# Kernel optimization log

Measured on AMD Instinct MI355X. Metric: run time of the kernel, lower is better.

Reference implementation:

```python
import jax, jax.numpy as jnp
import numpy as np

B, T, F, H, L = 256, 512, 64, 256, 2
DH = 2 * H          # decoder hidden size (bidirectional encoder concat)
OUT, OSL = 2, 20    # output_size, output_seq_len


def gru_cell(x, h, Wih, Whh, bih, bhh):
    # PyTorch GRU cell, gate order (r, z, n)
    gi = x @ Wih.T + bih
    gh = h @ Whh.T + bhh
    ir, iz, inn = jnp.split(gi, 3, axis=-1)
    hr, hz, hn = jnp.split(gh, 3, axis=-1)
    r = jax.nn.sigmoid(ir + hr)
    z = jax.nn.sigmoid(iz + hz)
    n = jnp.tanh(inn + r * hn)
    return (1.0 - z) * n + z * h


def setup_inputs() -> dict:
    key = jax.random.key(0)
    ks = iter(jax.random.split(key, 32))
    def p(shape, scale=0.05):
        return jax.random.normal(next(ks), shape, dtype=jnp.float32) * scale
    inp = {
        "x": p((B, T, F), 1.0),
        "start_token": jnp.zeros((1, 1, OUT), jnp.float32),
        # encoder layer 0 (input F), layer 1 (input 2H); axis 0 = direction (fwd, bwd)
        "enc_Wih0": p((2, 3 * H, F)), "enc_Whh0": p((2, 3 * H, H)),
        "enc_bih0": p((2, 3 * H)),   "enc_bhh0": p((2, 3 * H)),
        "enc_Wih1": p((2, 3 * H, 2 * H)), "enc_Whh1": p((2, 3 * H, H)),
        "enc_bih1": p((2, 3 * H)),   "enc_bhh1": p((2, 3 * H)),
        # decoder: unidirectional, hidden DH; layer0 input OUT, layer1 input DH
        "dec_Wih0": p((3 * DH, OUT)), "dec_Whh0": p((3 * DH, DH)),
        "dec_bih0": p((3 * DH,)),    "dec_bhh0": p((3 * DH,)),
        "dec_Wih1": p((3 * DH, DH)), "dec_Whh1": p((3 * DH, DH)),
        "dec_bih1": p((3 * DH,)),    "dec_bhh1": p((3 * DH,)),
        "fc_W": p((OUT, DH)), "fc_b": p((OUT,)),
    }
    return inp


def _run_dir(xs, Wih, Whh, bih, bhh, reverse):
    # xs: [T, B, Fin] -> (ys [T, B, H], h_T [B, H])
    h0 = jnp.zeros((xs.shape[1], Whh.shape[1]), xs.dtype)
    def step(h, xt):
        hn = gru_cell(xt, h, Wih, Whh, bih, bhh)
        return hn, hn
    hT, ys = jax.lax.scan(step, h0, xs, reverse=reverse)
    return ys, hT


def reference(x, start_token,
              enc_Wih0, enc_Whh0, enc_bih0, enc_bhh0,
              enc_Wih1, enc_Whh1, enc_bih1, enc_bhh1,
              dec_Wih0, dec_Whh0, dec_bih0, dec_bhh0,
              dec_Wih1, dec_Whh1, dec_bih1, dec_bhh1,
              fc_W, fc_b):
    b = x.shape[0]
    xs = jnp.swapaxes(x, 0, 1)  # [T, B, F]
    enc_layers = [(enc_Wih0, enc_Whh0, enc_bih0, enc_bhh0),
                  (enc_Wih1, enc_Whh1, enc_bih1, enc_bhh1)]
    hiddens = []
    layer_in = xs
    for (Wih, Whh, bih, bhh) in enc_layers:
        yf, hf = _run_dir(layer_in, Wih[0], Whh[0], bih[0], bhh[0], reverse=False)
        yb, hb = _run_dir(layer_in, Wih[1], Whh[1], bih[1], bhh[1], reverse=True)
        layer_in = jnp.concatenate([yf, yb], axis=-1)   # [T, B, 2H]
        hiddens.append(jnp.concatenate([hf, hb], axis=-1))  # [B, 2H] = cat(fwd, bwd)
    inp0 = jnp.broadcast_to(start_token, (b, 1, OUT))[:, 0]  # [B, OUT]
    def dec_step(carry, _):
        inp, (h0, h1) = carry
        h0n = gru_cell(inp, h0, dec_Wih0, dec_Whh0, dec_bih0, dec_bhh0)
        h1n = gru_cell(h0n, h1, dec_Wih1, dec_Whh1, dec_bih1, dec_bhh1)
        pred = h1n @ fc_W.T + fc_b
        return (pred, (h0n, h1n)), pred
    _, preds = jax.lax.scan(dec_step, (inp0, (hiddens[0], hiddens[1])), None, length=OSL)
    return jnp.swapaxes(preds, 0, 1)  # [B, OSL, OUT]
```

## Files before the change

### kernel.cpp

```cpp
#include <hip/hip_runtime.h>
#include <hip/hip_bf16.h>
#include <stdint.h>
#include <stddef.h>


typedef __bf16 bf16_t;
typedef bf16_t bf16x8 __attribute__((ext_vector_type(8)));
typedef float  f32x4  __attribute__((ext_vector_type(4)));

#define B_   256
#define T_   512
#define F_   64
#define H_   256
#define G_   768
#define DH_  512
#define DG_  1536
#define OSL_ 20

__device__ __forceinline__ float sigm(float x) {
    float e = __builtin_amdgcn_exp2f(-1.442695040888963f * x);
    return __builtin_amdgcn_rcpf(1.0f + e);
}
__device__ __forceinline__ float tanh_(float x) {
    float e = __builtin_amdgcn_exp2f(-2.885390081777927f * x);
    return __builtin_amdgcn_rcpf(1.0f + e) * 2.0f - 1.0f;
}

__device__ __forceinline__ bf16x8 load_f32x8_as_bf16(const float* p) {
    f32x4 u = *(const f32x4*)p;
    f32x4 v = *(const f32x4*)(p + 4);
    bf16x8 r;
    r[0]=(bf16_t)u[0]; r[1]=(bf16_t)u[1]; r[2]=(bf16_t)u[2]; r[3]=(bf16_t)u[3];
    r[4]=(bf16_t)v[0]; r[5]=(bf16_t)v[1]; r[6]=(bf16_t)v[2]; r[7]=(bf16_t)v[3];
    return r;
}

__global__ __launch_bounds__(256) void prep_all(
    const float* __restrict__ s0, const float* __restrict__ s1,
    const float* __restrict__ s2, const float* __restrict__ s3,
    const float* __restrict__ s4, const float* __restrict__ s5,
    const float* __restrict__ s6,
    bf16_t* __restrict__ d0, bf16_t* __restrict__ d1, bf16_t* __restrict__ d2,
    bf16_t* __restrict__ d3, bf16_t* __restrict__ d4, bf16_t* __restrict__ d5,
    bf16_t* __restrict__ d6,
    const float* __restrict__ wih0d, const float* __restrict__ fcw,
    const float* __restrict__ fcb, const float* __restrict__ bih0d,
    const float* __restrict__ st, bf16_t* __restrict__ weff,
    float* __restrict__ beff, float* __restrict__ ov,
    unsigned int* __restrict__ bar) {
    int i = blockIdx.x * 256 + threadIdx.x;
    switch (blockIdx.y) {
      case 0: if (i < 2*G_*F_)  d0[i] = (bf16_t)s0[i]; break;
      case 1: if (i < 2*G_*H_)  d1[i] = (bf16_t)s1[i]; break;
      case 2: if (i < 2*G_*DH_) d2[i] = (bf16_t)s2[i]; break;
      case 3: if (i < 2*G_*H_)  d3[i] = (bf16_t)s3[i]; break;
      case 4: if (i < DG_*DH_)  d4[i] = (bf16_t)s4[i]; break;
      case 5: if (i < DG_*DH_)  d5[i] = (bf16_t)s5[i]; break;
      case 6: if (i < DG_*DH_)  d6[i] = (bf16_t)s6[i]; break;
      default: {
        if (i < 1024) bar[i] = 0u;
        if (i < DG_*DH_) {
          int g = i >> 9, k = i & 511;
          float a0 = wih0d[g * 2], a1 = wih0d[g * 2 + 1];
          weff[i] = (bf16_t)(a0 * fcw[k] + a1 * fcw[DH_ + k]);
          if (k == 0) {
            beff[g] = a0 * fcb[0] + a1 * fcb[1] + bih0d[g];
            ov[g]   = a0 * st[0]  + a1 * st[1]  + bih0d[g];
          }
        }
      } break;
    }
}

__global__ __launch_bounds__(256) void gemm_gi(
    const float* __restrict__ x, const bf16_t* __restrict__ xcat,
    const bf16_t* __restrict__ Bt, bf16_t* __restrict__ gi, int t0, int K) {
    __shared__ bf16_t As[128 * 64];
    __shared__ bf16_t Bs[128 * 64];
    int m0 = blockIdx.x * 128, n0 = blockIdx.y * 128;
    int tid = threadIdx.x;
    int lane = tid & 63, w = tid >> 6;
    int col = lane & 15, quad = lane >> 4;
    int qm = (w >> 1) * 64, qn = (w & 1) * 64;

    int tl = m0 >> 8;
    int bbase = m0 & 255;
    int t_real = t0 + tl;
    if (n0 >= 768) t_real = (T_ - 1) - t_real;

    f32x4 acc[4][4] = {};
    for (int k0 = 0; k0 < K; k0 += 64) {
        __syncthreads();
#pragma unroll
        for (int i = 0; i < 4; i++) {
            int c = i * 256 + tid;
            int m = c >> 3, kc = c & 7;
            int kcs = kc ^ (m & 7);
            bf16x8 av;
            if (K == 64) {
                av = load_f32x8_as_bf16(x + ((size_t)(bbase + m) * T_ + t_real) * F_ + kcs * 8);
            } else {
                av = *(const bf16x8*)(xcat + ((size_t)t_real * B_ + bbase + m) * DH_ + k0 + kcs * 8);
            }
            *(bf16x8*)(&As[c * 8]) = av;
            *(bf16x8*)(&Bs[c * 8]) = *(const bf16x8*)(Bt + (size_t)(n0 + m) * K + k0 + kcs * 8);
        }
        __syncthreads();
#pragma unroll
        for (int kt = 0; kt < 2; kt++) {
            bf16x8 a[4], b[4];
#pragma unroll
            for (int mt = 0; mt < 4; mt++) {
                int r = qm + mt * 16 + col;
                a[mt] = *(const bf16x8*)(&As[(r * 8 + ((kt * 4 + quad) ^ (r & 7))) * 8]);
                int rn = qn + mt * 16 + col;
                b[mt] = *(const bf16x8*)(&Bs[(rn * 8 + ((kt * 4 + quad) ^ (rn & 7))) * 8]);
            }
#pragma unroll
            for (int mt = 0; mt < 4; mt++)
#pragma unroll
                for (int nt = 0; nt < 4; nt++)
                    acc[mt][nt] = __builtin_amdgcn_mfma_f32_16x16x32_bf16(a[mt], b[nt], acc[mt][nt], 0, 0, 0);
        }
    }
#pragma unroll
    for (int mt = 0; mt < 4; mt++)
#pragma unroll
        for (int nt = 0; nt < 4; nt++)
#pragma unroll
            for (int i = 0; i < 4; i++) {
                int row = m0 + qm + mt * 16 + quad * 4 + i;
                int cg  = n0 + qn + nt * 16 + col;
                gi[(size_t)row * DG_ + cg] = (bf16_t)acc[mt][nt][i];
            }
}

__global__ __launch_bounds__(512) void gru_scan(
    const bf16_t* __restrict__ gi, int t0, int tc,
    const bf16_t* __restrict__ whh,
    const float* __restrict__ bih, const float* __restrict__ bhh,
    float* __restrict__ hstate, bf16_t* __restrict__ y, float* __restrict__ hT) {
    __shared__ bf16_t gi_lds[16 * 768];
    __shared__ bf16_t h_lds[2 * 16 * 264];

    int dir = blockIdx.x >> 4;
    int b0  = (blockIdx.x & 15) * 16;
    int tid = threadIdx.x;
    int w = tid >> 6, lane = tid & 63, col = lane & 15, quad = lane >> 4;

    bf16x8 wf[3][2][8];
    const bf16_t* wbase = whh + (size_t)dir * G_ * H_;
#pragma unroll
    for (int g = 0; g < 3; g++)
#pragma unroll
        for (int nt = 0; nt < 2; nt++) {
            int row = g * 256 + w * 32 + nt * 16 + col;
#pragma unroll
            for (int kt = 0; kt < 8; kt++)
                wf[g][nt][kt] = *(const bf16x8*)(wbase + (size_t)row * H_ + kt * 32 + quad * 8);
        }
    float brz[2][2], bin_[2], bhn[2];
#pragma unroll
    for (int nt = 0; nt < 2; nt++) {
        int j = w * 32 + nt * 16 + col;
        brz[0][nt] = bih[dir * G_ + j] + bhh[dir * G_ + j];
        brz[1][nt] = bih[dir * G_ + 256 + j] + bhh[dir * G_ + 256 + j];
        bin_[nt]   = bih[dir * G_ + 512 + j];
        bhn[nt]    = bhh[dir * G_ + 512 + j];
    }
    int bb[3], oo[3];
#pragma unroll
    for (int it = 0; it < 3; it++) {
        int c = it * 512 + tid;
        bb[it] = c / 96;
        oo[it] = (c % 96) * 8;
    }
    float hold[2][4];
#pragma unroll
    for (int nt = 0; nt < 2; nt++)
#pragma unroll
        for (int i = 0; i < 4; i++) {
            int j = w * 32 + nt * 16 + col;
            hold[nt][i] = t0 ? hstate[dir * 65536 + (b0 + quad * 4 + i) * 256 + j] : 0.0f;
        }
    for (int i = tid; i < 16 * 264; i += 512) {
        int b = i / 264, j = i % 264;
        float v = (t0 && j < 256) ? hstate[dir * 65536 + (b0 + b) * 256 + j] : 0.0f;
        h_lds[i] = (bf16_t)v;
    }
#pragma unroll
    for (int it = 0; it < 3; it++) {
        int c = it * 512 + tid;
        *(bf16x8*)(&gi_lds[c * 8]) =
            *(const bf16x8*)(gi + ((size_t)0 * B_ + b0 + bb[it]) * DG_ + dir * G_ + oo[it]);
    }
    __syncthreads();

    for (int s = 0; s < tc; s++) {
        int par = s & 1;
        int t = t0 + s;
        int sn = (s + 1 < tc) ? (s + 1) : s;

        bf16x8 pg[3];
#pragma unroll
        for (int it = 0; it < 3; it++)
            pg[it] = *(const bf16x8*)(gi + ((size_t)sn * B_ + b0 + bb[it]) * DG_ + dir * G_ + oo[it]);

        f32x4 acc[3][2] = {};
        const bf16_t* hcur = &h_lds[par * 4224];
#pragma unroll
        for (int kt = 0; kt < 8; kt++) {
            bf16x8 af = *(const bf16x8*)(hcur + col * 264 + kt * 32 + quad * 8);
#pragma unroll
            for (int g = 0; g < 3; g++)
#pragma unroll
                for (int nt = 0; nt < 2; nt++)
                    acc[g][nt] = __builtin_amdgcn_mfma_f32_16x16x32_bf16(af, wf[g][nt][kt], acc[g][nt], 0, 0, 0);
        }

        bf16_t* hnext = &h_lds[(par ^ 1) * 4224];
        int tp = dir ? (T_ - 1 - t) : t;
#pragma unroll
        for (int nt = 0; nt < 2; nt++) {
            int j = w * 32 + nt * 16 + col;
#pragma unroll
            for (int i = 0; i < 4; i++) {
                int b = quad * 4 + i;
                float gr = acc[0][nt][i] + (float)gi_lds[b * 768 + j]       + brz[0][nt];
                float gz = acc[1][nt][i] + (float)gi_lds[b * 768 + 256 + j] + brz[1][nt];
                float gn = (float)gi_lds[b * 768 + 512 + j] + bin_[nt];
                float r = sigm(gr), z = sigm(gz);
                float n = tanh_(gn + r * (acc[2][nt][i] + bhn[nt]));
                float hv = (1.0f - z) * n + z * hold[nt][i];
                hold[nt][i] = hv;
                hnext[b * 264 + j] = (bf16_t)hv;
                if (t == T_ - 1) hT[(size_t)(b0 + b) * DH_ + dir * H_ + j] = hv;
            }
        }
        __syncthreads();
        if (y) {
            int b = tid >> 5, seg = tid & 31;
            *(bf16x8*)(y + ((size_t)tp * B_ + b0 + b) * DH_ + dir * H_ + seg * 8) =
                *(const bf16x8*)(&h_lds[(par ^ 1) * 4224 + b * 264 + seg * 8]);
        }
#pragma unroll
        for (int it = 0; it < 3; it++)
            *(bf16x8*)(&gi_lds[(it * 512 + tid) * 8]) = pg[it];
        __syncthreads();
    }
#pragma unroll
    for (int nt = 0; nt < 2; nt++)
#pragma unroll
        for (int i = 0; i < 4; i++) {
            int j = w * 32 + nt * 16 + col;
            hstate[dir * 65536 + (b0 + quad * 4 + i) * 256 + j] = hold[nt][i];
        }
}


__device__ __forceinline__ void gbar(unsigned int* cnt) {
    __syncthreads();
    if (threadIdx.x == 0) {
        __hip_atomic_fetch_add(cnt, 1u, __ATOMIC_RELEASE, __HIP_MEMORY_SCOPE_AGENT);
        unsigned int s = 0;
        while (__hip_atomic_load(cnt, __ATOMIC_RELAXED, __HIP_MEMORY_SCOPE_AGENT) < 8u
               && ++s < (1u << 20))
            __builtin_amdgcn_s_sleep(2);
    }
    __syncthreads();
}

__device__ __forceinline__ void stage16(bf16_t* lds, const bf16_t* src) {
    const char* s = (const char*)src;
    char* d = (char*)lds;
#pragma unroll
    for (int i2 = 0; i2 < 8; ++i2) {
        int off = i2 * 2048 + threadIdx.x * 8;
        unsigned long long v = __hip_atomic_load(
            (const unsigned long long*)(s + off),
            __ATOMIC_RELAXED, __HIP_MEMORY_SCOPE_AGENT);
        int row = off >> 10;
        int swz = off ^ ((row & 7) << 4);
        *(unsigned long long*)(d + swz) = v;
    }
}

__device__ __forceinline__ bf16x8 fragrd(const bf16_t* lds, int kt, int col, int quad) {
    int byte = (col * 1024 + kt * 64 + quad * 16) ^ ((col & 7) << 4);
    return *(const bf16x8*)((const char*)lds + byte);
}

__device__ __forceinline__ void publish(bf16_t* dst, int b, int j, float hv, int col) {
    bf16_t hb = (bf16_t)hv;
    unsigned short mb;
    __builtin_memcpy(&mb, &hb, 2);
    unsigned int pv = (unsigned int)__shfl_xor((int)(unsigned int)mb, 1);
    if ((col & 1) == 0) {
        unsigned int word = (unsigned int)mb | (pv << 16);
        __hip_atomic_store((unsigned int*)((char*)dst + (size_t)(b * DH_ + j) * 2),
                           word, __ATOMIC_RELAXED, __HIP_MEMORY_SCOPE_AGENT);
    }
}

__device__ __forceinline__ void cell_step(
    const bf16_t* sh, const bf16_t* sx, bool dox,
    const bf16_t* __restrict__ Wx, const bf16_t* __restrict__ Wh,
    int j, int col, int quad, int grp,
    float br, float bz, float bin_, float bhn,
    float hold[4], bf16_t* hout, float* hist_t) {
    f32x4 aR = {}, aZ = {}, aIN = {}, aHN = {};
#pragma unroll
    for (int kt = 0; kt < 16; ++kt) {
        bf16x8 ah = fragrd(sh, kt, col, quad);
        bf16x8 w0 = *(const bf16x8*)(Wh + (size_t)j * DH_ + kt * 32 + quad * 8);
        bf16x8 w1 = *(const bf16x8*)(Wh + (size_t)(DH_ + j) * DH_ + kt * 32 + quad * 8);
        bf16x8 w2 = *(const bf16x8*)(Wh + (size_t)(2 * DH_ + j) * DH_ + kt * 32 + quad * 8);
        aR  = __builtin_amdgcn_mfma_f32_16x16x32_bf16(ah, w0, aR, 0, 0, 0);
        aZ  = __builtin_amdgcn_mfma_f32_16x16x32_bf16(ah, w1, aZ, 0, 0, 0);
        aHN = __builtin_amdgcn_mfma_f32_16x16x32_bf16(ah, w2, aHN, 0, 0, 0);
        if (dox) {
            bf16x8 ax = fragrd(sx, kt, col, quad);
            bf16x8 x0 = *(const bf16x8*)(Wx + (size_t)j * DH_ + kt * 32 + quad * 8);
            bf16x8 x1 = *(const bf16x8*)(Wx + (size_t)(DH_ + j) * DH_ + kt * 32 + quad * 8);
            bf16x8 x2 = *(const bf16x8*)(Wx + (size_t)(2 * DH_ + j) * DH_ + kt * 32 + quad * 8);
            aR  = __builtin_amdgcn_mfma_f32_16x16x32_bf16(ax, x0, aR, 0, 0, 0);
            aZ  = __builtin_amdgcn_mfma_f32_16x16x32_bf16(ax, x1, aZ, 0, 0, 0);
            aIN = __builtin_amdgcn_mfma_f32_16x16x32_bf16(ax, x2, aIN, 0, 0, 0);
        }
    }
#pragma unroll
    for (int i = 0; i < 4; ++i) {
        int b = grp * 16 + quad * 4 + i;
        float r = sigm(aR[i] + br);
        float z = sigm(aZ[i] + bz);
        float n = tanh_(aIN[i] + bin_ + r * (aHN[i] + bhn));
        float hv = (1.0f - z) * n + z * hold[i];
        hold[i] = hv;
        if (hist_t) hist_t[(size_t)b * DH_ + j] = hv;
        publish(hout, b, j, hv, col);
    }
}

__global__ __launch_bounds__(256) void dec_persist(
    const bf16_t* __restrict__ weff, const float* __restrict__ beff,
    const float* __restrict__ ov,
    const bf16_t* __restrict__ wdhh0, const float* __restrict__ dbhh0,
    const bf16_t* __restrict__ wdih1, const float* __restrict__ dbih1,
    const bf16_t* __restrict__ wdhh1, const float* __restrict__ dbhh1,
    const float* __restrict__ h0init, const float* __restrict__ h1init,
    bf16_t* hx00, bf16_t* hx01, bf16_t* hx10, bf16_t* hx11,
    float* __restrict__ hist, unsigned int* __restrict__ bar) {
    __shared__ bf16_t sh[16 * 512];
    __shared__ bf16_t sx[16 * 512];
    int jblk = blockIdx.x & 7;
    int grp  = blockIdx.x >> 3;
    int tid = threadIdx.x, w = tid >> 6, lane = tid & 63;
    int col = lane & 15, quad = lane >> 4;
    int j = jblk * 64 + w * 16 + col;

    float b0r = beff[j] + dbhh0[j],           b0z = beff[DH_ + j] + dbhh0[DH_ + j];
    float b0in = beff[2 * DH_ + j],           b0hn = dbhh0[2 * DH_ + j];
    float o0r = ov[j] + dbhh0[j],             o0z = ov[DH_ + j] + dbhh0[DH_ + j];
    float o0in = ov[2 * DH_ + j];
    float b1r = dbih1[j] + dbhh1[j],          b1z = dbih1[DH_ + j] + dbhh1[DH_ + j];
    float b1in = dbih1[2 * DH_ + j],          b1hn = dbhh1[2 * DH_ + j];

    float hold0[4], hold1[4];
#pragma unroll
    for (int i = 0; i < 4; ++i) {
        int b = grp * 16 + quad * 4 + i;
        float v0 = h0init[(size_t)b * DH_ + j];
        float v1 = h1init[(size_t)b * DH_ + j];
        hold0[i] = v0; hold1[i] = v1;
        publish(hx01, b, j, v0, col);
        publish(hx11, b, j, v1, col);
    }
    gbar(bar + grp);

    int ph = 1;
    for (int t = 0; t < OSL_; ++t) {
        bf16_t* write0 = (t & 1) ? hx01 : hx00;
        bf16_t* read0  = (t & 1) ? hx00 : hx01;
        bf16_t* write1 = (t & 1) ? hx11 : hx10;
        bf16_t* read1  = (t & 1) ? hx10 : hx11;

        bool dox0 = (t > 0);
        __syncthreads();
        stage16(sh, read0 + (size_t)grp * 16 * DH_);
        if (dox0) stage16(sx, read1 + (size_t)grp * 16 * DH_);
        __syncthreads();
        cell_step(sh, sx, dox0, weff, wdhh0, j, col, quad, grp,
                  dox0 ? b0r : o0r, dox0 ? b0z : o0z, dox0 ? b0in : o0in, b0hn,
                  hold0, write0, nullptr);
        gbar(bar + ph * 16 + grp); ph++;

        __syncthreads();
        stage16(sh, read1 + (size_t)grp * 16 * DH_);
        stage16(sx, write0 + (size_t)grp * 16 * DH_);
        __syncthreads();
        cell_step(sh, sx, true, wdih1, wdhh1, j, col, quad, grp,
                  b1r, b1z, b1in, b1hn,
                  hold1, write1, hist + (size_t)t * B_ * DH_);
        gbar(bar + ph * 16 + grp); ph++;
    }
}

__global__ __launch_bounds__(256) void fc_all(
    const float* __restrict__ hist, const float* __restrict__ fcw,
    const float* __restrict__ fcb, float* __restrict__ out) {
    int t  = blockIdx.x >> 4;
    int b0 = (blockIdx.x & 15) * 16;
    int tid = threadIdx.x;
    int bl = tid >> 4, o = (tid >> 3) & 1, part = tid & 7;
    const float* hp = hist + ((size_t)t * B_ + b0 + bl) * DH_;
    const float* wp = fcw + o * DH_;
    float s = 0.0f;
    for (int k = part * 64; k < part * 64 + 64; k += 4) {
        f32x4 hv = *(const f32x4*)(hp + k);
        f32x4 wv = *(const f32x4*)(wp + k);
        s += hv[0] * wv[0] + hv[1] * wv[1] + hv[2] * wv[2] + hv[3] * wv[3];
    }
    s += __shfl_down(s, 4); s += __shfl_down(s, 2); s += __shfl_down(s, 1);
    if (part == 0) out[(size_t)(b0 + bl) * (OSL_ * 2) + t * 2 + o] = s + fcb[o];
}


#define OFF_WIH0E 0ull
#define OFF_WHH0E 196608ull
#define OFF_WIH1E 983040ull
#define OFF_WHH1E 2555904ull
#define OFF_WDHH0 3342336ull
#define OFF_WDIH1 4915200ull
#define OFF_WDHH1 6488064ull
#define OFF_WEFF  8060928ull
#define OFF_BEFF  9633792ull
#define OFF_BAR   9641984ull
#define OFF_OV    9658368ull
#define OFF_H0A   9682944ull
#define OFF_H0B   10207232ull
#define OFF_H1A   10731520ull
#define OFF_H1B   11255808ull
#define OFF_HST   11780096ull
#define OFF_HIST  12304384ull
#define OFF_XCAT  22790144ull
#define OFF_GI    157007872ull

extern "C" void kernel_launch(void* const* d_in, const int* in_sizes, int n_in,
                              void* d_out, int out_size, void* d_ws, size_t ws_size,
                              hipStream_t stream) {
    const float* x      = (const float*)d_in[0];
    const float* st     = (const float*)d_in[1];
    const float* eWih0  = (const float*)d_in[2];
    const float* eWhh0  = (const float*)d_in[3];
    const float* ebih0  = (const float*)d_in[4];
    const float* ebhh0  = (const float*)d_in[5];
    const float* eWih1  = (const float*)d_in[6];
    const float* eWhh1  = (const float*)d_in[7];
    const float* ebih1  = (const float*)d_in[8];
    const float* ebhh1  = (const float*)d_in[9];
    const float* dWih0  = (const float*)d_in[10];
    const float* dWhh0  = (const float*)d_in[11];
    const float* dbih0  = (const float*)d_in[12];
    const float* dbhh0  = (const float*)d_in[13];
    const float* dWih1  = (const float*)d_in[14];
    const float* dWhh1  = (const float*)d_in[15];
    const float* dbih1  = (const float*)d_in[16];
    const float* dbhh1  = (const float*)d_in[17];
    const float* fcW    = (const float*)d_in[18];
    const float* fcb    = (const float*)d_in[19];

    char* ws = (char*)d_ws;
    bf16_t* wih0e = (bf16_t*)(ws + OFF_WIH0E);
    bf16_t* whh0e = (bf16_t*)(ws + OFF_WHH0E);
    bf16_t* wih1e = (bf16_t*)(ws + OFF_WIH1E);
    bf16_t* whh1e = (bf16_t*)(ws + OFF_WHH1E);
    bf16_t* wdhh0 = (bf16_t*)(ws + OFF_WDHH0);
    bf16_t* wdih1 = (bf16_t*)(ws + OFF_WDIH1);
    bf16_t* wdhh1 = (bf16_t*)(ws + OFF_WDHH1);
    bf16_t* weff  = (bf16_t*)(ws + OFF_WEFF);
    float*  beff  = (float*)(ws + OFF_BEFF);
    unsigned int* bar = (unsigned int*)(ws + OFF_BAR);
    float*  ovp   = (float*)(ws + OFF_OV);
    float*  h0init = (float*)(ws + OFF_H0A);
    float*  h1init = (float*)(ws + OFF_H1A);
    bf16_t* hx00  = (bf16_t*)(ws + OFF_H0B);
    bf16_t* hx01  = (bf16_t*)(ws + OFF_H0B + 262144ull);
    bf16_t* hx10  = (bf16_t*)(ws + OFF_H1B);
    bf16_t* hx11  = (bf16_t*)(ws + OFF_H1B + 262144ull);
    float*  hstate = (float*)(ws + OFF_HST);
    float*  hist  = (float*)(ws + OFF_HIST);
    bf16_t* xcat  = (bf16_t*)(ws + OFF_XCAT);
    bf16_t* gi    = (bf16_t*)(ws + OFF_GI);

    int Tc = 512;
    while (Tc > 8 && OFF_GI + (unsigned long long)Tc * 786432ull > (unsigned long long)ws_size)
        Tc >>= 1;
    int nch = T_ / Tc;

    prep_all<<<dim3(3072, 8), 256, 0, stream>>>(
        eWih0, eWhh0, eWih1, eWhh1, dWhh0, dWih1, dWhh1,
        wih0e, whh0e, wih1e, whh1e, wdhh0, wdih1, wdhh1,
        dWih0, fcW, fcb, dbih0, st, weff, beff, ovp, bar);

    for (int c = 0; c < nch; c++) {
        gemm_gi<<<dim3(Tc * 2, 12), 256, 0, stream>>>(x, nullptr, wih0e, gi, c * Tc, 64);
        gru_scan<<<32, 512, 0, stream>>>(gi, c * Tc, Tc, whh0e, ebih0, ebhh0, hstate, xcat, h0init);
    }
    for (int c = 0; c < nch; c++) {
        gemm_gi<<<dim3(Tc * 2, 12), 256, 0, stream>>>(nullptr, xcat, wih1e, gi, c * Tc, 512);
        gru_scan<<<32, 512, 0, stream>>>(gi, c * Tc, Tc, whh1e, ebih1, ebhh1, hstate, nullptr, h1init);
    }

    dec_persist<<<128, 256, 0, stream>>>(weff, beff, ovp,
                                         wdhh0, dbhh0, wdih1, dbih1, wdhh1, dbhh1,
                                         h0init, h1init,
                                         hx00, hx01, hx10, hx11,
                                         hist, bar);

    fc_all<<<OSL_ * 16, 256, 0, stream>>>(hist, fcW, fcb, (float*)d_out);
}
```

Baseline: 5.067 ms.

## Hoist decoder layer-1 recurrent GEMM before barrier, swap GEMM grid axes, direct y stores

In the decoder, the layer-1 recurrent product (h1 times Whh1) only depends on the previous step, so it is now computed together with layer 0 before the first grid barrier. This shortens the critical path between barriers and drops one LDS staging of h1. The gi GEMM grid swaps its x and y axes so the N tiles vary fastest, which changes the block order for cache reuse of the A tiles. The encoder scan now writes y directly from registers as scalar bf16 stores instead of vectorized copies out of LDS, and the barrier spin sleep is shortened. Scalar scattered stores may use more memory transactions than the old vector copies.

```diff
diff --git a/kernel.cpp b/kernel.cpp
--- a/kernel.cpp
+++ b/kernel.cpp
@@ -77,7 +77,7 @@
     const bf16_t* __restrict__ Bt, bf16_t* __restrict__ gi, int t0, int K) {
     __shared__ bf16_t As[128 * 64];
     __shared__ bf16_t Bs[128 * 64];
-    int m0 = blockIdx.x * 128, n0 = blockIdx.y * 128;
+    int m0 = blockIdx.y * 128, n0 = blockIdx.x * 128;
     int tid = threadIdx.x;
     int lane = tid & 63, w = tid >> 6;
     int col = lane & 15, quad = lane >> 4;
@@ -234,15 +234,11 @@
                 float hv = (1.0f - z) * n + z * hold[nt][i];
                 hold[nt][i] = hv;
                 hnext[b * 264 + j] = (bf16_t)hv;
+                if (y) y[((size_t)tp * B_ + b0 + b) * DH_ + dir * H_ + j] = (bf16_t)hv;
                 if (t == T_ - 1) hT[(size_t)(b0 + b) * DH_ + dir * H_ + j] = hv;
             }
         }
         __syncthreads();
-        if (y) {
-            int b = tid >> 5, seg = tid & 31;
-            *(bf16x8*)(y + ((size_t)tp * B_ + b0 + b) * DH_ + dir * H_ + seg * 8) =
-                *(const bf16x8*)(&h_lds[(par ^ 1) * 4224 + b * 264 + seg * 8]);
-        }
 #pragma unroll
         for (int it = 0; it < 3; it++)
             *(bf16x8*)(&gi_lds[(it * 512 + tid) * 8]) = pg[it];
@@ -265,7 +261,7 @@
         unsigned int s = 0;
         while (__hip_atomic_load(cnt, __ATOMIC_RELAXED, __HIP_MEMORY_SCOPE_AGENT) < 8u
                && ++s < (1u << 20))
-            __builtin_amdgcn_s_sleep(2);
+            __builtin_amdgcn_s_sleep(1);
     }
     __syncthreads();
 }
@@ -299,45 +295,6 @@
         unsigned int word = (unsigned int)mb | (pv << 16);
         __hip_atomic_store((unsigned int*)((char*)dst + (size_t)(b * DH_ + j) * 2),
                            word, __ATOMIC_RELAXED, __HIP_MEMORY_SCOPE_AGENT);
-    }
-}
-
-__device__ __forceinline__ void cell_step(
-    const bf16_t* sh, const bf16_t* sx, bool dox,
-    const bf16_t* __restrict__ Wx, const bf16_t* __restrict__ Wh,
-    int j, int col, int quad, int grp,
-    float br, float bz, float bin_, float bhn,
-    float hold[4], bf16_t* hout, float* hist_t) {
-    f32x4 aR = {}, aZ = {}, aIN = {}, aHN = {};
-#pragma unroll
-    for (int kt = 0; kt < 16; ++kt) {
-        bf16x8 ah = fragrd(sh, kt, col, quad);
-        bf16x8 w0 = *(const bf16x8*)(Wh + (size_t)j * DH_ + kt * 32 + quad * 8);
-        bf16x8 w1 = *(const bf16x8*)(Wh + (size_t)(DH_ + j) * DH_ + kt * 32 + quad * 8);
-        bf16x8 w2 = *(const bf16x8*)(Wh + (size_t)(2 * DH_ + j) * DH_ + kt * 32 + quad * 8);
-        aR  = __builtin_amdgcn_mfma_f32_16x16x32_bf16(ah, w0, aR, 0, 0, 0);
-        aZ  = __builtin_amdgcn_mfma_f32_16x16x32_bf16(ah, w1, aZ, 0, 0, 0);
-        aHN = __builtin_amdgcn_mfma_f32_16x16x32_bf16(ah, w2, aHN, 0, 0, 0);
-        if (dox) {
-            bf16x8 ax = fragrd(sx, kt, col, quad);
-            bf16x8 x0 = *(const bf16x8*)(Wx + (size_t)j * DH_ + kt * 32 + quad * 8);
-            bf16x8 x1 = *(const bf16x8*)(Wx + (size_t)(DH_ + j) * DH_ + kt * 32 + quad * 8);
-            bf16x8 x2 = *(const bf16x8*)(Wx + (size_t)(2 * DH_ + j) * DH_ + kt * 32 + quad * 8);
-            aR  = __builtin_amdgcn_mfma_f32_16x16x32_bf16(ax, x0, aR, 0, 0, 0);
-            aZ  = __builtin_amdgcn_mfma_f32_16x16x32_bf16(ax, x1, aZ, 0, 0, 0);
-            aIN = __builtin_amdgcn_mfma_f32_16x16x32_bf16(ax, x2, aIN, 0, 0, 0);
-        }
-    }
-#pragma unroll
-    for (int i = 0; i < 4; ++i) {
-        int b = grp * 16 + quad * 4 + i;
-        float r = sigm(aR[i] + br);
-        float z = sigm(aZ[i] + bz);
-        float n = tanh_(aIN[i] + bin_ + r * (aHN[i] + bhn));
-        float hv = (1.0f - z) * n + z * hold[i];
-        hold[i] = hv;
-        if (hist_t) hist_t[(size_t)b * DH_ + j] = hv;
-        publish(hout, b, j, hv, col);
     }
 }
 
@@ -383,24 +340,79 @@
         bf16_t* read0  = (t & 1) ? hx00 : hx01;
         bf16_t* write1 = (t & 1) ? hx11 : hx10;
         bf16_t* read1  = (t & 1) ? hx10 : hx11;
-
         bool dox0 = (t > 0);
+
         __syncthreads();
         stage16(sh, read0 + (size_t)grp * 16 * DH_);
-        if (dox0) stage16(sx, read1 + (size_t)grp * 16 * DH_);
-        __syncthreads();
-        cell_step(sh, sx, dox0, weff, wdhh0, j, col, quad, grp,
-                  dox0 ? b0r : o0r, dox0 ? b0z : o0z, dox0 ? b0in : o0in, b0hn,
-                  hold0, write0, nullptr);
+        stage16(sx, read1 + (size_t)grp * 16 * DH_);
+        __syncthreads();
+
+        f32x4 aR0 = {}, aZ0 = {}, aHN0 = {}, aIN0 = {};
+        f32x4 aR1 = {}, aZ1 = {}, aHN1 = {};
+#pragma unroll
+        for (int kt = 0; kt < 16; ++kt) {
+            bf16x8 ah = fragrd(sh, kt, col, quad);
+            bf16x8 ax = fragrd(sx, kt, col, quad);
+            bf16x8 h0w0 = *(const bf16x8*)(wdhh0 + (size_t)j * DH_ + kt * 32 + quad * 8);
+            bf16x8 h0w1 = *(const bf16x8*)(wdhh0 + (size_t)(DH_ + j) * DH_ + kt * 32 + quad * 8);
+            bf16x8 h0w2 = *(const bf16x8*)(wdhh0 + (size_t)(2 * DH_ + j) * DH_ + kt * 32 + quad * 8);
+            aR0  = __builtin_amdgcn_mfma_f32_16x16x32_bf16(ah, h0w0, aR0, 0, 0, 0);
+            aZ0  = __builtin_amdgcn_mfma_f32_16x16x32_bf16(ah, h0w1, aZ0, 0, 0, 0);
+            aHN0 = __builtin_amdgcn_mfma_f32_16x16x32_bf16(ah, h0w2, aHN0, 0, 0, 0);
+            bf16x8 h1w0 = *(const bf16x8*)(wdhh1 + (size_t)j * DH_ + kt * 32 + quad * 8);
+            bf16x8 h1w1 = *(const bf16x8*)(wdhh1 + (size_t)(DH_ + j) * DH_ + kt * 32 + quad * 8);
+            bf16x8 h1w2 = *(const bf16x8*)(wdhh1 + (size_t)(2 * DH_ + j) * DH_ + kt * 32 + quad * 8);
+            aR1  = __builtin_amdgcn_mfma_f32_16x16x32_bf16(ax, h1w0, aR1, 0, 0, 0);
+            aZ1  = __builtin_amdgcn_mfma_f32_16x16x32_bf16(ax, h1w1, aZ1, 0, 0, 0);
+            aHN1 = __builtin_amdgcn_mfma_f32_16x16x32_bf16(ax, h1w2, aHN1, 0, 0, 0);
+            if (dox0) {
+                bf16x8 x0 = *(const bf16x8*)(weff + (size_t)j * DH_ + kt * 32 + quad * 8);
+                bf16x8 x1 = *(const bf16x8*)(weff + (size_t)(DH_ + j) * DH_ + kt * 32 + quad * 8);
+                bf16x8 x2 = *(const bf16x8*)(weff + (size_t)(2 * DH_ + j) * DH_ + kt * 32 + quad * 8);
+                aR0  = __builtin_amdgcn_mfma_f32_16x16x32_bf16(ax, x0, aR0, 0, 0, 0);
+                aZ0  = __builtin_amdgcn_mfma_f32_16x16x32_bf16(ax, x1, aZ0, 0, 0, 0);
+                aIN0 = __builtin_amdgcn_mfma_f32_16x16x32_bf16(ax, x2, aIN0, 0, 0, 0);
+            }
+        }
+#pragma unroll
+        for (int i = 0; i < 4; ++i) {
+            int b = grp * 16 + quad * 4 + i;
+            float r = sigm(aR0[i] + (dox0 ? b0r : o0r));
+            float z = sigm(aZ0[i] + (dox0 ? b0z : o0z));
+            float n = tanh_(aIN0[i] + (dox0 ? b0in : o0in) + r * (aHN0[i] + b0hn));
+            float hv = (1.0f - z) * n + z * hold0[i];
+            hold0[i] = hv;
+            publish(write0, b, j, hv, col);
+        }
         gbar(bar + ph * 16 + grp); ph++;
 
         __syncthreads();
-        stage16(sh, read1 + (size_t)grp * 16 * DH_);
         stage16(sx, write0 + (size_t)grp * 16 * DH_);
         __syncthreads();
-        cell_step(sh, sx, true, wdih1, wdhh1, j, col, quad, grp,
-                  b1r, b1z, b1in, b1hn,
-                  hold1, write1, hist + (size_t)t * B_ * DH_);
+
+        f32x4 aIN1 = {};
+#pragma unroll
+        for (int kt = 0; kt < 16; ++kt) {
+            bf16x8 a0 = fragrd(sx, kt, col, quad);
+            bf16x8 x0 = *(const bf16x8*)(wdih1 + (size_t)j * DH_ + kt * 32 + quad * 8);
+            bf16x8 x1 = *(const bf16x8*)(wdih1 + (size_t)(DH_ + j) * DH_ + kt * 32 + quad * 8);
+            bf16x8 x2 = *(const bf16x8*)(wdih1 + (size_t)(2 * DH_ + j) * DH_ + kt * 32 + quad * 8);
+            aR1  = __builtin_amdgcn_mfma_f32_16x16x32_bf16(a0, x0, aR1, 0, 0, 0);
+            aZ1  = __builtin_amdgcn_mfma_f32_16x16x32_bf16(a0, x1, aZ1, 0, 0, 0);
+            aIN1 = __builtin_amdgcn_mfma_f32_16x16x32_bf16(a0, x2, aIN1, 0, 0, 0);
+        }
+        float* hist_t = hist + (size_t)t * B_ * DH_;
+#pragma unroll
+        for (int i = 0; i < 4; ++i) {
+            int b = grp * 16 + quad * 4 + i;
+            float r = sigm(aR1[i] + b1r);
+            float z = sigm(aZ1[i] + b1z);
+            float n = tanh_(aIN1[i] + b1in + r * (aHN1[i] + b1hn));
+            float hv = (1.0f - z) * n + z * hold1[i];
+            hold1[i] = hv;
+            hist_t[(size_t)b * DH_ + j] = hv;
+            publish(write1, b, j, hv, col);
+        }
         gbar(bar + ph * 16 + grp); ph++;
     }
 }
@@ -503,11 +515,11 @@
         dWih0, fcW, fcb, dbih0, st, weff, beff, ovp, bar);
 
     for (int c = 0; c < nch; c++) {
-        gemm_gi<<<dim3(Tc * 2, 12), 256, 0, stream>>>(x, nullptr, wih0e, gi, c * Tc, 64);
+        gemm_gi<<<dim3(12, Tc * 2), 256, 0, stream>>>(x, nullptr, wih0e, gi, c * Tc, 64);
         gru_scan<<<32, 512, 0, stream>>>(gi, c * Tc, Tc, whh0e, ebih0, ebhh0, hstate, xcat, h0init);
     }
     for (int c = 0; c < nch; c++) {
-        gemm_gi<<<dim3(Tc * 2, 12), 256, 0, stream>>>(nullptr, xcat, wih1e, gi, c * Tc, 512);
+        gemm_gi<<<dim3(12, Tc * 2), 256, 0, stream>>>(nullptr, xcat, wih1e, gi, c * Tc, 512);
         gru_scan<<<32, 512, 0, stream>>>(gi, c * Tc, Tc, whh1e, ebih1, ebhh1, hstate, nullptr, h1init);
     }
 
```

After: 4.900 ms. 3.3% less time.
